# Kernel tuning notes

Hardware: AMD Instinct MI355X
Metric: run time of the kernel (lower is better)

Reference implementation:

```python
import jax, jax.numpy as jnp
import numpy as np

N_NODES = 100000
N_EDGES = 1600000
HIDDEN = 48
LAYERS = 4
ALPHA = 0.1
THETA = 0.5


def setup_inputs() -> dict:
    key = jax.random.key(0)
    ks = jax.random.split(key, 6)
    x = jax.random.normal(ks[0], (N_NODES, 3), dtype=jnp.float32)
    edge_index = jax.random.randint(ks[1], (2, N_EDGES), 0, N_NODES, dtype=jnp.int32)
    W0 = jax.random.normal(ks[2], (3, HIDDEN), dtype=jnp.float32) * 0.3
    b0 = jnp.zeros((HIDDEN,), dtype=jnp.float32)
    convW = jax.random.normal(ks[3], (LAYERS, HIDDEN, HIDDEN), dtype=jnp.float32) * (1.0 / np.sqrt(HIDDEN))
    W1 = jax.random.normal(ks[4], (HIDDEN, HIDDEN), dtype=jnp.float32) * (1.0 / np.sqrt(HIDDEN))
    b1 = jnp.zeros((HIDDEN,), dtype=jnp.float32)
    return {"x": x, "edge_index": edge_index, "W0": W0, "b0": b0,
            "convW": convW, "W1": W1, "b1": b1}


def reference(x, edge_index, W0, b0, convW, W1, b1):
    # lin0 + relu; x0 is the initial residual (dropout=0 / eval mode -> identity)
    h = jax.nn.relu(x @ W0 + b0)
    x0 = h
    src, dst = edge_index[0], edge_index[1]
    n = h.shape[0]
    for l in range(LAYERS):
        # sparse propagation: A @ h via gather + segment_sum (unit edge weights, normalize=False)
        agg = jax.ops.segment_sum(h[src], dst, num_segments=n)
        beta = float(np.log(THETA / (l + 1) + 1.0))
        # GCNII shared-weights branch: t = (1-alpha)*Ah + alpha*x0; out = (1-beta)*t + beta*(t @ W)
        t = (1.0 - ALPHA) * agg + ALPHA * x0
        h = jax.nn.relu((1.0 - beta) * t + beta * (t @ convW[l]))
    out = h @ W1 + b1
    return jax.nn.log_softmax(out, axis=-1)
```

## Files before the change

kernel.cpp:

```cpp
#include <hip/hip_runtime.h>
#include <math.h>

#define N_NODES 100000
#define N_EDGES 1600000
#define HID 48
#define HPAD 64
#define ALPHA 0.1f

typedef unsigned short u16;
typedef unsigned int u32;

__device__ __forceinline__ float bf_lo(u32 u) { return __uint_as_float(u << 16); }
__device__ __forceinline__ float bf_hi(u32 u) { return __uint_as_float(u & 0xffff0000u); }
__device__ __forceinline__ float bf2f(u16 u) {
    return __uint_as_float(((u32)u) << 16);
}
__device__ __forceinline__ u16 f2bf(float f) {
    u32 b = __float_as_uint(f);
    b += 0x7fff + ((b >> 16) & 1);
    return (u16)(b >> 16);
}
__device__ __forceinline__ u32 pack2(float a, float b) {
    return (u32)f2bf(a) | ((u32)f2bf(b) << 16);
}

__global__ __launch_bounds__(256) void lin0_k(const float* __restrict__ x, const float* __restrict__ W0,
                                              const float* __restrict__ b0, u16* __restrict__ h0) {
    int t = blockIdx.x * 256 + threadIdx.x;
    if (t >= N_NODES * 6) return;
    int node = t / 6, oct = t % 6;
    float xv0 = x[node * 3 + 0], xv1 = x[node * 3 + 1], xv2 = x[node * 3 + 2];
    float v[8];
#pragma unroll
    for (int j = 0; j < 8; j++) {
        int f = oct * 8 + j;
        float s = b0[f] + xv0 * W0[0 * HID + f] + xv1 * W0[1 * HID + f] + xv2 * W0[2 * HID + f];
        v[j] = s > 0.f ? s : 0.f;
    }
    uint4 p;
    p.x = pack2(v[0], v[1]); p.y = pack2(v[2], v[3]);
    p.z = pack2(v[4], v[5]); p.w = pack2(v[6], v[7]);
    *(uint4*)(h0 + (size_t)node * HPAD + oct * 8) = p;
}

__global__ __launch_bounds__(256) void count_k(const int* __restrict__ dst, int* __restrict__ deg,
                                               int* __restrict__ rank) {
    int e = blockIdx.x * 256 + threadIdx.x;
    if (e < N_EDGES) rank[e] = atomicAdd(&deg[dst[e]], 1);
}

__global__ __launch_bounds__(256) void scan1_k(const int* __restrict__ deg, int* __restrict__ rowptr,
                                               int* __restrict__ partial) {
    __shared__ int sums[256];
    int tid = threadIdx.x;
    int base = blockIdx.x * 2048 + tid * 8;
    int v[8]; int s = 0;
#pragma unroll
    for (int j = 0; j < 8; j++) { int idx = base + j; v[j] = (idx < N_NODES) ? deg[idx] : 0; s += v[j]; }
    sums[tid] = s; __syncthreads();
    for (int off = 1; off < 256; off <<= 1) {
        int t = (tid >= off) ? sums[tid - off] : 0;
        __syncthreads();
        sums[tid] += t;
        __syncthreads();
    }
    if (tid == 255) partial[blockIdx.x] = sums[255];
    int run = (tid > 0) ? sums[tid - 1] : 0;
#pragma unroll
    for (int j = 0; j < 8; j++) { int idx = base + j; if (idx < N_NODES) rowptr[idx] = run; run += v[j]; }
}

__global__ void scan2_k(int* __restrict__ partial, int* __restrict__ rowptr, int nblk) {
    int lane = threadIdx.x & 63;
    int v = (lane < nblk) ? partial[lane] : 0;
    for (int off = 1; off < 64; off <<= 1) {
        int t = __shfl_up(v, off);
        if (lane >= off) v += t;
    }
    int excl = __shfl_up(v, 1);
    if (lane == 0) excl = 0;
    if (lane < nblk) partial[lane] = excl;
    if (lane == 63) rowptr[N_NODES] = v;
}

__global__ __launch_bounds__(256) void scan3_k(int* __restrict__ rowptr, const int* __restrict__ partial) {
    int tid = threadIdx.x;
    int base = blockIdx.x * 2048 + tid * 8;
    int add = partial[blockIdx.x];
#pragma unroll
    for (int j = 0; j < 8; j++) {
        int idx = base + j;
        if (idx < N_NODES) rowptr[idx] += add;
    }
}

__global__ __launch_bounds__(256) void bucket_k(const int* __restrict__ src, const int* __restrict__ dst,
                                                const int* __restrict__ rank, const int* __restrict__ rowptr,
                                                int* __restrict__ ssrc) {
    int e = blockIdx.x * 256 + threadIdx.x;
    if (e < N_EDGES) {
        int d = dst[e];
        ssrc[rowptr[d] + rank[e]] = src[e];
    }
}

__global__ __launch_bounds__(256) void layer_k(const u16* __restrict__ h_in, const u16* __restrict__ x0,
                                               const int* __restrict__ rowptr, const int* __restrict__ ssrc,
                                               const float* __restrict__ W, float beta,
                                               u16* __restrict__ h_out) {
    __shared__ float sW[2304];
    __shared__ float tbuf[4][48];
    int tid = threadIdx.x, wave = tid >> 6, lane = tid & 63;
#pragma unroll
    for (int i = 0; i < 9; i++) sW[i * 256 + tid] = W[i * 256 + tid];
    int node = blockIdx.x * 4 + wave;
    int chunk = lane & 7;
    int slot  = lane >> 3;
    bool act = chunk < 6;
    int cc = act ? chunk : 0;
    float a0 = 0.f, a1 = 0.f, a2 = 0.f, a3 = 0.f, a4 = 0.f, a5 = 0.f, a6 = 0.f, a7 = 0.f;
    if (node < N_NODES) {
        int e0 = rowptr[node], e1 = rowptr[node + 1];
        int e = e0;
        for (; e + 16 <= e1; e += 16) {
            int sA = ssrc[e + slot];
            int sB = ssrc[e + 8 + slot];
            const uint4 wA = *(const uint4*)(h_in + ((size_t)sA << 6) + cc * 8);
            const uint4 wB = *(const uint4*)(h_in + ((size_t)sB << 6) + cc * 8);
            a0 += bf_lo(wA.x) + bf_lo(wB.x);
            a1 += bf_hi(wA.x) + bf_hi(wB.x);
            a2 += bf_lo(wA.y) + bf_lo(wB.y);
            a3 += bf_hi(wA.y) + bf_hi(wB.y);
            a4 += bf_lo(wA.z) + bf_lo(wB.z);
            a5 += bf_hi(wA.z) + bf_hi(wB.z);
            a6 += bf_lo(wA.w) + bf_lo(wB.w);
            a7 += bf_hi(wA.w) + bf_hi(wB.w);
        }
        for (; e < e1; e += 8) {
            int idx = e + slot;
            int s = ssrc[idx < e1 ? idx : e];
            const uint4 w = *(const uint4*)(h_in + ((size_t)s << 6) + cc * 8);
            if (idx < e1) {
                a0 += bf_lo(w.x); a1 += bf_hi(w.x);
                a2 += bf_lo(w.y); a3 += bf_hi(w.y);
                a4 += bf_lo(w.z); a5 += bf_hi(w.z);
                a6 += bf_lo(w.w); a7 += bf_hi(w.w);
            }
        }
#pragma unroll
        for (int off = 8; off <= 32; off <<= 1) {
            a0 += __shfl_xor(a0, off); a1 += __shfl_xor(a1, off);
            a2 += __shfl_xor(a2, off); a3 += __shfl_xor(a3, off);
            a4 += __shfl_xor(a4, off); a5 += __shfl_xor(a5, off);
            a6 += __shfl_xor(a6, off); a7 += __shfl_xor(a7, off);
        }
        if (act && slot == 0) {
            const uint4 xv = *(const uint4*)(x0 + ((size_t)node << 6) + chunk * 8);
            float4 t0, t1;
            t0.x = (1.f - ALPHA) * a0 + ALPHA * bf_lo(xv.x);
            t0.y = (1.f - ALPHA) * a1 + ALPHA * bf_hi(xv.x);
            t0.z = (1.f - ALPHA) * a2 + ALPHA * bf_lo(xv.y);
            t0.w = (1.f - ALPHA) * a3 + ALPHA * bf_hi(xv.y);
            t1.x = (1.f - ALPHA) * a4 + ALPHA * bf_lo(xv.z);
            t1.y = (1.f - ALPHA) * a5 + ALPHA * bf_hi(xv.z);
            t1.z = (1.f - ALPHA) * a6 + ALPHA * bf_lo(xv.w);
            t1.w = (1.f - ALPHA) * a7 + ALPHA * bf_hi(xv.w);
            ((float4*)tbuf[wave])[chunk * 2 + 0] = t0;
            ((float4*)tbuf[wave])[chunk * 2 + 1] = t1;
        }
    }
    __syncthreads();
    if (node < N_NODES && lane < 48) {
        const float4* t4 = (const float4*)tbuf[wave];
        float s = 0.f;
#pragma unroll
        for (int k4 = 0; k4 < 12; k4++) {
            float4 tv = t4[k4];
            s += tv.x * sW[(4 * k4 + 0) * 48 + lane] + tv.y * sW[(4 * k4 + 1) * 48 + lane]
               + tv.z * sW[(4 * k4 + 2) * 48 + lane] + tv.w * sW[(4 * k4 + 3) * 48 + lane];
        }
        float t = tbuf[wave][lane];
        float o = (1.f - beta) * t + beta * s;
        h_out[(size_t)node * HPAD + lane] = f2bf(o > 0.f ? o : 0.f);
    }
}

__global__ __launch_bounds__(256) void final_k(const u16* __restrict__ h, const float* __restrict__ W1,
                                               const float* __restrict__ b1, float* __restrict__ out) {
    __shared__ float sW[2304];
    __shared__ float sb[48];
    __shared__ float tbuf[4][48];
    int tid = threadIdx.x, wave = tid >> 6, lane = tid & 63;
#pragma unroll
    for (int i = 0; i < 9; i++) sW[i * 256 + tid] = W1[i * 256 + tid];
    if (tid < 48) sb[tid] = b1[tid];
    int node = blockIdx.x * 4 + wave;
    int f = lane < 48 ? lane : 0;
    if (node < N_NODES && lane < 48) tbuf[wave][lane] = bf2f(h[(size_t)node * HPAD + lane]);
    __syncthreads();
    float v = -INFINITY;
    if (node < N_NODES) {
        const float4* t4 = (const float4*)tbuf[wave];
        float s = sb[f];
#pragma unroll
        for (int k4 = 0; k4 < 12; k4++) {
            float4 tv = t4[k4];
            s += tv.x * sW[(4 * k4 + 0) * 48 + f] + tv.y * sW[(4 * k4 + 1) * 48 + f]
               + tv.z * sW[(4 * k4 + 2) * 48 + f] + tv.w * sW[(4 * k4 + 3) * 48 + f];
        }
        if (lane < 48) v = s;
    }
    float m = v;
    for (int off = 32; off >= 1; off >>= 1) m = fmaxf(m, __shfl_xor(m, off));
    float ex = (node < N_NODES && lane < 48) ? expf(v - m) : 0.f;
    float sum = ex;
    for (int off = 32; off >= 1; off >>= 1) sum += __shfl_xor(sum, off);
    if (node < N_NODES && lane < 48) {
        out[node * 48 + lane] = v - m - logf(sum);
    }
}

extern "C" void kernel_launch(void* const* d_in, const int* in_sizes, int n_in,
                              void* d_out, int out_size, void* d_ws, size_t ws_size,
                              hipStream_t stream) {
    const float* x     = (const float*)d_in[0];
    const int*   ei    = (const int*)d_in[1];
    const float* W0    = (const float*)d_in[2];
    const float* b0    = (const float*)d_in[3];
    const float* convW = (const float*)d_in[4];
    const float* W1    = (const float*)d_in[5];
    const float* b1    = (const float*)d_in[6];
    float* out = (float*)d_out;
    const int* src = ei;
    const int* dst = ei + N_EDGES;

    char* ws = (char*)d_ws;
    size_t off = 0;
    u16* h0 = (u16*)(ws + off); off += (size_t)N_NODES * HPAD * 2;
    u16* hA = (u16*)(ws + off); off += (size_t)N_NODES * HPAD * 2;
    u16* hB = (u16*)(ws + off); off += (size_t)N_NODES * HPAD * 2;
    int* rank = (int*)hA;
    int* ssrc = (int*)(ws + off);   off += (size_t)N_EDGES * 4;
    int* rowptr = (int*)(ws + off); off += (size_t)(N_NODES + 1) * 4;
    off = (off + 255) & ~(size_t)255;
    int* deg = (int*)(ws + off);    off += (size_t)N_NODES * 4;
    off = (off + 255) & ~(size_t)255;
    int* partial = (int*)(ws + off); off += 64 * 4;

    hipMemsetAsync(deg, 0, (size_t)N_NODES * 4, stream);

    lin0_k<<<(N_NODES * 6 + 255) / 256, 256, 0, stream>>>(x, W0, b0, h0);
    count_k<<<6250, 256, 0, stream>>>(dst, deg, rank);
    scan1_k<<<49, 256, 0, stream>>>(deg, rowptr, partial);
    scan2_k<<<1, 64, 0, stream>>>(partial, rowptr, 49);
    scan3_k<<<49, 256, 0, stream>>>(rowptr, partial);
    bucket_k<<<6250, 256, 0, stream>>>(src, dst, rank, rowptr, ssrc);

    const float betas[4] = { logf(1.5f), logf(1.25f), logf(7.f / 6.f), logf(1.125f) };

    layer_k<<<25000, 256, 0, stream>>>(h0, h0, rowptr, ssrc, convW + 0 * 2304, betas[0], hB);
    layer_k<<<25000, 256, 0, stream>>>(hB, h0, rowptr, ssrc, convW + 1 * 2304, betas[1], hA);
    layer_k<<<25000, 256, 0, stream>>>(hA, h0, rowptr, ssrc, convW + 2 * 2304, betas[2], hB);
    layer_k<<<25000, 256, 0, stream>>>(hB, h0, rowptr, ssrc, convW + 3 * 2304, betas[3], hA);
    final_k<<<25000, 256, 0, stream>>>(hA, W1, b1, out);
}
```

Before: 512.0 us.

## Persistent waves with register-resident weights and readlane matvec in layer/final kernels

The layer and final kernels become persistent: 1536 blocks loop over nodes, and each lane keeps one column of the 48x48 weight matrix in registers, loaded once per block, instead of reloading W into LDS per 4-node block. The beta blend and identity term are folded into a single matrix M = beta*W + (1-beta)*I. The gather now uses 4 edge slots by 12 feature chunks of 4 bf16 values, reduced with DPP quad ops, and the matvec broadcasts t values via readlane instead of LDS plus __syncthreads. This removes per-block weight staging and barriers, but the 48-float register array raises VGPR pressure and reduces edge-level parallelism per wave.

New measurement: 676.6 us. +32.1%, slower.

```diff
diff --git a/kernel.cpp b/kernel.cpp
--- a/kernel.cpp
+++ b/kernel.cpp
@@ -7,14 +7,15 @@
 #define HPAD 64
 #define ALPHA 0.1f
 
+#define LBLK 1536
+#define LWAVES (LBLK * 4)
+#define NPW ((N_NODES + LWAVES - 1) / LWAVES)
+
 typedef unsigned short u16;
 typedef unsigned int u32;
 
 __device__ __forceinline__ float bf_lo(u32 u) { return __uint_as_float(u << 16); }
 __device__ __forceinline__ float bf_hi(u32 u) { return __uint_as_float(u & 0xffff0000u); }
-__device__ __forceinline__ float bf2f(u16 u) {
-    return __uint_as_float(((u32)u) << 16);
-}
 __device__ __forceinline__ u16 f2bf(float f) {
     u32 b = __float_as_uint(f);
     b += 0x7fff + ((b >> 16) & 1);
@@ -23,6 +24,10 @@
 __device__ __forceinline__ u32 pack2(float a, float b) {
     return (u32)f2bf(a) | ((u32)f2bf(b) << 16);
 }
+
+#define QXOR1(x) __int_as_float(__builtin_amdgcn_update_dpp(0, __float_as_int(x), 0xB1, 0xF, 0xF, false))
+#define QXOR2(x) __int_as_float(__builtin_amdgcn_update_dpp(0, __float_as_int(x), 0x4E, 0xF, 0xF, false))
+#define RLANE(x, l) __int_as_float(__builtin_amdgcn_readlane(__float_as_int(x), (l)))
 
 __global__ __launch_bounds__(256) void lin0_k(const float* __restrict__ x, const float* __restrict__ W0,
                                               const float* __restrict__ b0, u16* __restrict__ h0) {
@@ -108,115 +113,111 @@
                                                const int* __restrict__ rowptr, const int* __restrict__ ssrc,
                                                const float* __restrict__ W, float beta,
                                                u16* __restrict__ h_out) {
-    __shared__ float sW[2304];
-    __shared__ float tbuf[4][48];
-    int tid = threadIdx.x, wave = tid >> 6, lane = tid & 63;
-#pragma unroll
-    for (int i = 0; i < 9; i++) sW[i * 256 + tid] = W[i * 256 + tid];
-    int node = blockIdx.x * 4 + wave;
-    int chunk = lane & 7;
-    int slot  = lane >> 3;
-    bool act = chunk < 6;
-    int cc = act ? chunk : 0;
-    float a0 = 0.f, a1 = 0.f, a2 = 0.f, a3 = 0.f, a4 = 0.f, a5 = 0.f, a6 = 0.f, a7 = 0.f;
-    if (node < N_NODES) {
+    __shared__ float sM[2304];
+    int tid = threadIdx.x, lane = tid & 63;
+    for (int i = tid; i < 2304; i += 256) {
+        int r = i / 48, c = i - r * 48;
+        float v = beta * W[i];
+        if (r == c) v += 1.f - beta;
+        sM[i] = v;
+    }
+    __syncthreads();
+    int f = lane < 48 ? lane : 0;
+    float wreg[48];
+#pragma unroll
+    for (int r = 0; r < 48; ++r) wreg[r] = sM[r * 48 + f];
+
+    int slot = lane & 3;
+    int chunk = lane >> 2;
+    int cc = chunk < 12 ? chunk : 0;
+    int wid = blockIdx.x * 4 + (tid >> 6);
+
+    for (int i = 0; i < NPW; ++i) {
+        int node = wid + i * LWAVES;
+        if (node >= N_NODES) break;
         int e0 = rowptr[node], e1 = rowptr[node + 1];
+        float a0 = 0.f, a1 = 0.f, a2 = 0.f, a3 = 0.f;
         int e = e0;
         for (; e + 16 <= e1; e += 16) {
             int sA = ssrc[e + slot];
-            int sB = ssrc[e + 8 + slot];
-            const uint4 wA = *(const uint4*)(h_in + ((size_t)sA << 6) + cc * 8);
-            const uint4 wB = *(const uint4*)(h_in + ((size_t)sB << 6) + cc * 8);
-            a0 += bf_lo(wA.x) + bf_lo(wB.x);
-            a1 += bf_hi(wA.x) + bf_hi(wB.x);
-            a2 += bf_lo(wA.y) + bf_lo(wB.y);
-            a3 += bf_hi(wA.y) + bf_hi(wB.y);
-            a4 += bf_lo(wA.z) + bf_lo(wB.z);
-            a5 += bf_hi(wA.z) + bf_hi(wB.z);
-            a6 += bf_lo(wA.w) + bf_lo(wB.w);
-            a7 += bf_hi(wA.w) + bf_hi(wB.w);
-        }
-        for (; e < e1; e += 8) {
+            int sB = ssrc[e + 4 + slot];
+            int sC = ssrc[e + 8 + slot];
+            int sD = ssrc[e + 12 + slot];
+            const uint2 wA = *(const uint2*)(h_in + ((size_t)sA << 6) + cc * 4);
+            const uint2 wB = *(const uint2*)(h_in + ((size_t)sB << 6) + cc * 4);
+            const uint2 wC = *(const uint2*)(h_in + ((size_t)sC << 6) + cc * 4);
+            const uint2 wD = *(const uint2*)(h_in + ((size_t)sD << 6) + cc * 4);
+            a0 += (bf_lo(wA.x) + bf_lo(wB.x)) + (bf_lo(wC.x) + bf_lo(wD.x));
+            a1 += (bf_hi(wA.x) + bf_hi(wB.x)) + (bf_hi(wC.x) + bf_hi(wD.x));
+            a2 += (bf_lo(wA.y) + bf_lo(wB.y)) + (bf_lo(wC.y) + bf_lo(wD.y));
+            a3 += (bf_hi(wA.y) + bf_hi(wB.y)) + (bf_hi(wC.y) + bf_hi(wD.y));
+        }
+        for (; e < e1; e += 4) {
             int idx = e + slot;
             int s = ssrc[idx < e1 ? idx : e];
-            const uint4 w = *(const uint4*)(h_in + ((size_t)s << 6) + cc * 8);
+            const uint2 w = *(const uint2*)(h_in + ((size_t)s << 6) + cc * 4);
             if (idx < e1) {
                 a0 += bf_lo(w.x); a1 += bf_hi(w.x);
                 a2 += bf_lo(w.y); a3 += bf_hi(w.y);
-                a4 += bf_lo(w.z); a5 += bf_hi(w.z);
-                a6 += bf_lo(w.w); a7 += bf_hi(w.w);
             }
         }
-#pragma unroll
-        for (int off = 8; off <= 32; off <<= 1) {
-            a0 += __shfl_xor(a0, off); a1 += __shfl_xor(a1, off);
-            a2 += __shfl_xor(a2, off); a3 += __shfl_xor(a3, off);
-            a4 += __shfl_xor(a4, off); a5 += __shfl_xor(a5, off);
-            a6 += __shfl_xor(a6, off); a7 += __shfl_xor(a7, off);
-        }
-        if (act && slot == 0) {
-            const uint4 xv = *(const uint4*)(x0 + ((size_t)node << 6) + chunk * 8);
-            float4 t0, t1;
-            t0.x = (1.f - ALPHA) * a0 + ALPHA * bf_lo(xv.x);
-            t0.y = (1.f - ALPHA) * a1 + ALPHA * bf_hi(xv.x);
-            t0.z = (1.f - ALPHA) * a2 + ALPHA * bf_lo(xv.y);
-            t0.w = (1.f - ALPHA) * a3 + ALPHA * bf_hi(xv.y);
-            t1.x = (1.f - ALPHA) * a4 + ALPHA * bf_lo(xv.z);
-            t1.y = (1.f - ALPHA) * a5 + ALPHA * bf_hi(xv.z);
-            t1.z = (1.f - ALPHA) * a6 + ALPHA * bf_lo(xv.w);
-            t1.w = (1.f - ALPHA) * a7 + ALPHA * bf_hi(xv.w);
-            ((float4*)tbuf[wave])[chunk * 2 + 0] = t0;
-            ((float4*)tbuf[wave])[chunk * 2 + 1] = t1;
-        }
-    }
-    __syncthreads();
-    if (node < N_NODES && lane < 48) {
-        const float4* t4 = (const float4*)tbuf[wave];
-        float s = 0.f;
-#pragma unroll
-        for (int k4 = 0; k4 < 12; k4++) {
-            float4 tv = t4[k4];
-            s += tv.x * sW[(4 * k4 + 0) * 48 + lane] + tv.y * sW[(4 * k4 + 1) * 48 + lane]
-               + tv.z * sW[(4 * k4 + 2) * 48 + lane] + tv.w * sW[(4 * k4 + 3) * 48 + lane];
-        }
-        float t = tbuf[wave][lane];
-        float o = (1.f - beta) * t + beta * s;
-        h_out[(size_t)node * HPAD + lane] = f2bf(o > 0.f ? o : 0.f);
+        a0 += QXOR1(a0); a0 += QXOR2(a0);
+        a1 += QXOR1(a1); a1 += QXOR2(a1);
+        a2 += QXOR1(a2); a2 += QXOR2(a2);
+        a3 += QXOR1(a3); a3 += QXOR2(a3);
+        const uint2 xv = *(const uint2*)(x0 + ((size_t)node << 6) + cc * 4);
+        a0 = (1.f - ALPHA) * a0 + ALPHA * bf_lo(xv.x);
+        a1 = (1.f - ALPHA) * a1 + ALPHA * bf_hi(xv.x);
+        a2 = (1.f - ALPHA) * a2 + ALPHA * bf_lo(xv.y);
+        a3 = (1.f - ALPHA) * a3 + ALPHA * bf_hi(xv.y);
+        float p0 = 0.f, p1 = 0.f, p2 = 0.f, p3 = 0.f;
+#pragma unroll
+        for (int c = 0; c < 12; ++c) {
+            p0 = fmaf(RLANE(a0, 4 * c), wreg[4 * c + 0], p0);
+            p1 = fmaf(RLANE(a1, 4 * c), wreg[4 * c + 1], p1);
+            p2 = fmaf(RLANE(a2, 4 * c), wreg[4 * c + 2], p2);
+            p3 = fmaf(RLANE(a3, 4 * c), wreg[4 * c + 3], p3);
+        }
+        float o = (p0 + p1) + (p2 + p3);
+        if (lane < 48) h_out[((size_t)node << 6) + lane] = f2bf(o > 0.f ? o : 0.f);
     }
 }
 
 __global__ __launch_bounds__(256) void final_k(const u16* __restrict__ h, const float* __restrict__ W1,
                                                const float* __restrict__ b1, float* __restrict__ out) {
     __shared__ float sW[2304];
-    __shared__ float sb[48];
-    __shared__ float tbuf[4][48];
-    int tid = threadIdx.x, wave = tid >> 6, lane = tid & 63;
-#pragma unroll
-    for (int i = 0; i < 9; i++) sW[i * 256 + tid] = W1[i * 256 + tid];
-    if (tid < 48) sb[tid] = b1[tid];
-    int node = blockIdx.x * 4 + wave;
+    int tid = threadIdx.x, lane = tid & 63;
+    for (int i = tid; i < 2304; i += 256) sW[i] = W1[i];
+    __syncthreads();
     int f = lane < 48 ? lane : 0;
-    if (node < N_NODES && lane < 48) tbuf[wave][lane] = bf2f(h[(size_t)node * HPAD + lane]);
-    __syncthreads();
-    float v = -INFINITY;
-    if (node < N_NODES) {
-        const float4* t4 = (const float4*)tbuf[wave];
-        float s = sb[f];
-#pragma unroll
-        for (int k4 = 0; k4 < 12; k4++) {
-            float4 tv = t4[k4];
-            s += tv.x * sW[(4 * k4 + 0) * 48 + f] + tv.y * sW[(4 * k4 + 1) * 48 + f]
-               + tv.z * sW[(4 * k4 + 2) * 48 + f] + tv.w * sW[(4 * k4 + 3) * 48 + f];
-        }
-        if (lane < 48) v = s;
-    }
-    float m = v;
-    for (int off = 32; off >= 1; off >>= 1) m = fmaxf(m, __shfl_xor(m, off));
-    float ex = (node < N_NODES && lane < 48) ? expf(v - m) : 0.f;
-    float sum = ex;
-    for (int off = 32; off >= 1; off >>= 1) sum += __shfl_xor(sum, off);
-    if (node < N_NODES && lane < 48) {
-        out[node * 48 + lane] = v - m - logf(sum);
+    float wreg[48];
+#pragma unroll
+    for (int r = 0; r < 48; ++r) wreg[r] = sW[r * 48 + f];
+    float bv = b1[f];
+    int chunk = lane >> 2;
+    int cc = chunk < 12 ? chunk : 0;
+    int wid = blockIdx.x * 4 + (tid >> 6);
+
+    for (int i = 0; i < NPW; ++i) {
+        int node = wid + i * LWAVES;
+        if (node >= N_NODES) break;
+        const uint2 hv = *(const uint2*)(h + ((size_t)node << 6) + cc * 4);
+        float a0 = bf_lo(hv.x), a1 = bf_hi(hv.x), a2 = bf_lo(hv.y), a3 = bf_hi(hv.y);
+        float p0 = bv, p1 = 0.f, p2 = 0.f, p3 = 0.f;
+#pragma unroll
+        for (int c = 0; c < 12; ++c) {
+            p0 = fmaf(RLANE(a0, 4 * c), wreg[4 * c + 0], p0);
+            p1 = fmaf(RLANE(a1, 4 * c), wreg[4 * c + 1], p1);
+            p2 = fmaf(RLANE(a2, 4 * c), wreg[4 * c + 2], p2);
+            p3 = fmaf(RLANE(a3, 4 * c), wreg[4 * c + 3], p3);
+        }
+        float v = (lane < 48) ? (p0 + p1) + (p2 + p3) : -INFINITY;
+        float m = v;
+        for (int off = 32; off >= 1; off >>= 1) m = fmaxf(m, __shfl_xor(m, off));
+        float ex = (lane < 48) ? expf(v - m) : 0.f;
+        float sum = ex;
+        for (int off = 32; off >= 1; off >>= 1) sum += __shfl_xor(sum, off);
+        if (lane < 48) out[(size_t)node * 48 + lane] = v - m - logf(sum);
     }
 }
 
@@ -258,9 +259,9 @@
 
     const float betas[4] = { logf(1.5f), logf(1.25f), logf(7.f / 6.f), logf(1.125f) };
 
-    layer_k<<<25000, 256, 0, stream>>>(h0, h0, rowptr, ssrc, convW + 0 * 2304, betas[0], hB);
-    layer_k<<<25000, 256, 0, stream>>>(hB, h0, rowptr, ssrc, convW + 1 * 2304, betas[1], hA);
-    layer_k<<<25000, 256, 0, stream>>>(hA, h0, rowptr, ssrc, convW + 2 * 2304, betas[2], hB);
-    layer_k<<<25000, 256, 0, stream>>>(hB, h0, rowptr, ssrc, convW + 3 * 2304, betas[3], hA);
-    final_k<<<25000, 256, 0, stream>>>(hA, W1, b1, out);
-}
+    layer_k<<<LBLK, 256, 0, stream>>>(h0, h0, rowptr, ssrc, convW + 0 * 2304, betas[0], hB);
+    layer_k<<<LBLK, 256, 0, stream>>>(hB, h0, rowptr, ssrc, convW + 1 * 2304, betas[1], hA);
+    layer_k<<<LBLK, 256, 0, stream>>>(hA, h0, rowptr, ssrc, convW + 2 * 2304, betas[2], hB);
+    layer_k<<<LBLK, 256, 0, stream>>>(hB, h0, rowptr, ssrc, convW + 3 * 2304, betas[3], hA);
+    final_k<<<LBLK, 256, 0, stream>>>(hA, W1, b1, out);
+}
```
